# Optimization experiments

Hardware: AMD Instinct MI355X
Metric: run time of the kernel (lower is better)

## Reference

```python
import jax, jax.numpy as jnp
import numpy as np

NUM_STAGES = 8
NUM_CODEBOOKS = 1024  # 2**10
DATA_DIM = 256
T = 131072


def setup_inputs() -> dict:
    key = jax.random.key(0)
    k_x, k_cb = jax.random.split(key)
    input_data = jax.random.normal(k_x, (T, DATA_DIM), dtype=jnp.float32)
    # torch init: Uniform(-1/K, 1/K) per stage
    bound = 1.0 / NUM_CODEBOOKS
    codebooks = jax.random.uniform(
        k_cb, (NUM_STAGES, NUM_CODEBOOKS, DATA_DIM), dtype=jnp.float32,
        minval=-bound, maxval=bound)
    return {"input_data": input_data, "codebooks": codebooks}


def _hard_vq(residual, cb):
    dists = (jnp.sum(residual * residual, axis=1, keepdims=True)
             - 2.0 * (residual @ cb.T)
             + jnp.sum(cb * cb, axis=1)[None, :])
    idx = jnp.argmin(dists, axis=1)          # [T]
    q = cb[idx]                               # gather -> [T, D]
    return q, residual - q, idx


def reference(input_data, codebooks):
    # eval path: stage_map=None (mask of ones), train_mode=False
    residual = input_data
    recon = jnp.zeros_like(input_data)
    mses = []
    for i in range(codebooks.shape[0]):  # fixed small stage loop
        q, residual, _ = _hard_vq(residual, codebooks[i])
        recon = recon + q  # intermediate reconstruction = cumulative sum of q
        mses.append(jnp.mean((recon - input_data) ** 2))
    final_output = recon
    return final_output, jnp.stack(mses)
```

## Files before the change

kernel.cpp:

```cpp
#include <hip/hip_runtime.h>
#include <stdint.h>


#define T_ROWS   131072
#define DIM      256
#define NSTAGE   8
#define NCB      1024
#define WROWS    64
#define BLK_ROWS 256
#define NTHREADS 256
#define CHUNK_CW 32
#define NCHUNK   (NCB / CHUNK_CW)
#define CHUNK_BYTES (CHUNK_CW * 512)

#define WS_CB_BYTES    (NSTAGE * NCB * 512)
#define WS_CNORM_OFF   WS_CB_BYTES
#define WS_CNORM_BYTES (NSTAGE * NCB * 4)
#define WS_MSE_OFF     (WS_CNORM_OFF + WS_CNORM_BYTES)
#define WS_IDX_OFF     (WS_MSE_OFF + 64)

typedef __attribute__((ext_vector_type(8)))  short  s16x8;
typedef __attribute__((ext_vector_type(8)))  __bf16 bf16x8;
typedef __attribute__((ext_vector_type(4)))  float  f32x4;
typedef __attribute__((ext_vector_type(16))) float  f32x16;

__device__ __forceinline__ unsigned short f2bf(float f) {
  union { float f; unsigned u; } v; v.f = f;
  unsigned r = v.u + 0x7FFFu + ((v.u >> 16) & 1u);
  return (unsigned short)(r >> 16);
}

__global__ void vq_prep(const float* __restrict__ CB, char* __restrict__ wscb,
                        float* __restrict__ cnorm) {
  const int tid = threadIdx.x;
  const int cwl = tid >> 5;
  const int j   = tid & 31;
  const int cw  = blockIdx.x * 8 + cwl;
  const int c   = cw & (NCB - 1);
  const float* src = CB + (size_t)cw * DIM + 8 * j;
  f32x4 a = *(const f32x4*)(src);
  f32x4 b = *(const f32x4*)(src + 4);
  s16x8 h;
#pragma unroll
  for (int e = 0; e < 4; ++e) { h[e] = (short)f2bf(a[e]); h[4 + e] = (short)f2bf(b[e]); }
  float sq = a[0]*a[0] + a[1]*a[1] + a[2]*a[2] + a[3]*a[3]
           + b[0]*b[0] + b[1]*b[1] + b[2]*b[2] + b[3]*b[3];
#pragma unroll
  for (int m = 1; m <= 16; m <<= 1) sq += __shfl_xor(sq, m);
  *(s16x8*)(wscb + (size_t)cw * 512 + ((16 * j) ^ ((c & 31) << 4))) = h;
  if (j == 0) cnorm[cw] = sq;
}

__global__ __launch_bounds__(NTHREADS, 2)
void vq_search(const float* __restrict__ X,
               const char* __restrict__ wscb, const float* __restrict__ cnorm,
               unsigned short* __restrict__ IDX, float* __restrict__ wsmse) {
  __shared__ __align__(16) char  lds_cb[3][CHUNK_BYTES];
  __shared__ __align__(16) float lds_cn[NCB];
  __shared__ int   lds_idx[BLK_ROWS];
  __shared__ float lds_n[BLK_ROWS];

  const int tid  = threadIdx.x;
  const int wave = tid >> 6;
  const int lane = tid & 63;
  const int c32  = lane & 31;
  const int hi   = lane >> 5;

  const int rowbase = blockIdx.x * BLK_ROWS + wave * WROWS;

  bf16x8 af[2][16];
  float  sq[2];
#pragma unroll
  for (int t = 0; t < 2; ++t) {
    const float* px = X + (size_t)(rowbase + t * 32 + c32) * DIM + 8 * hi;
    float s2 = 0.f;
#pragma unroll
    for (int s = 0; s < 16; ++s) {
      f32x4 a = *(const f32x4*)(px + 16 * s);
      f32x4 b = *(const f32x4*)(px + 16 * s + 4);
      bf16x8 tt;
#pragma unroll
      for (int e = 0; e < 4; ++e) {
        tt[e] = (__bf16)a[e]; tt[4 + e] = (__bf16)b[e];
        s2 += a[e] * a[e] + b[e] * b[e];
      }
      af[t][s] = tt;
    }
    sq[t] = s2;
  }
#pragma unroll
  for (int t = 0; t < 2; ++t) {
    float v = sq[t] + __shfl_xor(sq[t], 32);
    if (lane < 32) lds_n[wave * WROWS + t * 32 + c32] = v;
  }

  __builtin_amdgcn_global_load_lds(
      (const __attribute__((address_space(1))) char*)((const char*)cnorm + wave * 1024 + lane * 16),
      (__attribute__((address_space(3))) char*)((char*)lds_cn + wave * 1024),
      16, 0, 0);
#pragma unroll
  for (int ch = 0; ch < 2; ++ch)
#pragma unroll
    for (int i = 0; i < 4; ++i) {
      const int seg = (wave * 4 + i) * 1024;
      __builtin_amdgcn_global_load_lds(
          (const __attribute__((address_space(1))) char*)(wscb + (size_t)ch * CHUNK_BYTES + seg + lane * 16),
          (__attribute__((address_space(3))) char*)(&lds_cb[ch][0] + seg),
          16, 0, 0);
    }

  const int swz = c32 << 4;

#pragma unroll 1
  for (int st = 0; st < NSTAGE; ++st) {
    float mv0[16], mv1[16];
#pragma unroll
    for (int r = 0; r < 16; ++r) { mv0[r] = -3.402823466e38f; mv1[r] = -3.402823466e38f; }

    const char* stage_cb = wscb + (size_t)st * NCB * 512;

#pragma unroll 1
    for (int ch = 0; ch < NCHUNK; ++ch) {
      const int cur = ch % 3;

      if (ch + 2 < NCHUNK) {
        const int nx = (ch + 2) % 3;
        const char* src = stage_cb + (size_t)(ch + 2) * CHUNK_BYTES;
#pragma unroll
        for (int i = 0; i < 4; ++i) {
          const int seg = (wave * 4 + i) * 1024;
          __builtin_amdgcn_global_load_lds(
              (const __attribute__((address_space(1))) char*)(src + seg + lane * 16),
              (__attribute__((address_space(3))) char*)(&lds_cb[nx][0] + seg),
              16, 0, 0);
        }
        asm volatile("s_waitcnt vmcnt(8)" ::: "memory");
      } else if (ch + 1 < NCHUNK) {
        asm volatile("s_waitcnt vmcnt(4)" ::: "memory");
      } else {
        asm volatile("s_waitcnt vmcnt(0)" ::: "memory");
      }
      __builtin_amdgcn_sched_barrier(0);
      __builtin_amdgcn_s_barrier();
      __builtin_amdgcn_sched_barrier(0);

      const float cn = lds_cn[ch * CHUNK_CW + c32];
      const float ci = -0.5f * cn;
      f32x16 acc0, acc1;
#pragma unroll
      for (int r = 0; r < 16; ++r) { acc0[r] = ci; acc1[r] = ci; }

      const char* buf = &lds_cb[cur][0];
#pragma unroll
      for (int s = 0; s < 16; ++s) {
        bf16x8 b = *(const bf16x8*)(buf + c32 * 512 + ((s * 32 + hi * 16) ^ swz));
        acc0 = __builtin_amdgcn_mfma_f32_32x32x16_bf16(af[0][s], b, acc0, 0, 0, 0);
        acc1 = __builtin_amdgcn_mfma_f32_32x32x16_bf16(af[1][s], b, acc1, 0, 0, 0);
      }

      const unsigned col = (unsigned)(ch * CHUNK_CW + c32);
#pragma unroll
      for (int r = 0; r < 16; ++r) {
        union { float f; unsigned u; } p0, p1;
        p0.f = acc0[r]; p0.u = (p0.u & 0xFFFFFC00u) | col;
        p1.f = acc1[r]; p1.u = (p1.u & 0xFFFFFC00u) | col;
        mv0[r] = fmaxf(mv0[r], p0.f);
        mv1[r] = fmaxf(mv1[r], p1.f);
      }
      __builtin_amdgcn_sched_barrier(0);
      __builtin_amdgcn_s_barrier();
    }

    float msum = 0.f;
#pragma unroll
    for (int t = 0; t < 2; ++t)
#pragma unroll
      for (int r = 0; r < 16; ++r) {
        float v = (t == 0) ? mv0[r] : mv1[r];
#pragma unroll
        for (int m = 1; m <= 16; m <<= 1) v = fmaxf(v, __shfl_xor(v, m));
        union { float f; unsigned u; } w; w.f = v;
        const float vtrue = __builtin_bit_cast(float, w.u & 0xFFFFFC00u);
        const int   row   = t * 32 + (r & 3) + 8 * (r >> 2) + 4 * hi;
        const int   wrow  = wave * WROWS + row;
        const float n_new = lds_n[wrow] - 2.0f * vtrue;
        msum += n_new;
        if (c32 == 0) {
          lds_n[wrow]   = n_new;
          const int ix = (int)(w.u & 1023u);
          lds_idx[wrow] = ix;
          IDX[st * T_ROWS + rowbase + row] = (unsigned short)ix;
        }
      }
    msum += __shfl_xor(msum, 32);
    if (lane == 0) atomicAdd(wsmse + st, msum);

    if (st != NSTAGE - 1) {
      const char* ncb = stage_cb + (size_t)NCB * 512;
      const char* ncn = (const char*)cnorm + (size_t)(st + 1) * NCB * 4;
      __builtin_amdgcn_global_load_lds(
          (const __attribute__((address_space(1))) char*)(ncn + wave * 1024 + lane * 16),
          (__attribute__((address_space(3))) char*)((char*)lds_cn + wave * 1024),
          16, 0, 0);
#pragma unroll
      for (int ch = 0; ch < 2; ++ch)
#pragma unroll
        for (int i = 0; i < 4; ++i) {
          const int seg = (wave * 4 + i) * 1024;
          __builtin_amdgcn_global_load_lds(
              (const __attribute__((address_space(1))) char*)(ncb + (size_t)ch * CHUNK_BYTES + seg + lane * 16),
              (__attribute__((address_space(3))) char*)(&lds_cb[ch][0] + seg),
              16, 0, 0);
        }

#pragma unroll
      for (int t = 0; t < 2; ++t) {
        const int idx = lds_idx[wave * WROWS + t * 32 + c32];
        const char* q = stage_cb + (size_t)idx * 512;
        const int swzu = (idx & 31) << 4;
#pragma unroll
        for (int s = 0; s < 16; ++s) {
          bf16x8 qb = *(const bf16x8*)(q + ((s * 32 + hi * 16) ^ swzu));
          bf16x8 tt = af[t][s];
#pragma unroll
          for (int e = 0; e < 8; ++e)
            tt[e] = (__bf16)((float)tt[e] - (float)qb[e]);
          af[t][s] = tt;
        }
      }
    }
  }
}

__global__ __launch_bounds__(256)
void vq_recon(const char* __restrict__ wscb, const unsigned short* __restrict__ IDX,
              float* __restrict__ OUT) {
  const int tid = threadIdx.x;
  const int row = blockIdx.x * (256 / 8) + (tid >> 3);
  const int g   = tid & 7;

  int idxs[NSTAGE];
#pragma unroll
  for (int st = 0; st < NSTAGE; ++st) idxs[st] = IDX[st * T_ROWS + row];

  float a[32];
#pragma unroll
  for (int d = 0; d < 32; ++d) a[d] = 0.f;

#pragma unroll
  for (int st = 0; st < NSTAGE; ++st) {
    const char* q = wscb + ((size_t)st * NCB + idxs[st]) * 512;
    const int swzu = (idxs[st] & 31) << 4;
#pragma unroll
    for (int k = 0; k < 4; ++k) {
      bf16x8 qb = *(const bf16x8*)(q + ((g * 64 + 16 * k) ^ swzu));
#pragma unroll
      for (int e = 0; e < 8; ++e) a[k * 8 + e] += (float)qb[e];
    }
  }

  float* po = OUT + (size_t)row * DIM + g * 32;
#pragma unroll
  for (int m = 0; m < 8; ++m) {
    f32x4 o = {a[4 * m], a[4 * m + 1], a[4 * m + 2], a[4 * m + 3]};
    *(f32x4*)(po + 4 * m) = o;
  }
}

__global__ void vq_fin(const float* __restrict__ wsmse, float* __restrict__ OUT) {
  const int i = threadIdx.x;
  if (i < NSTAGE) {
    OUT[(size_t)T_ROWS * DIM + i] = wsmse[i] * (1.0f / ((float)T_ROWS * (float)DIM));
  }
}

extern "C" void kernel_launch(void* const* d_in, const int* in_sizes, int n_in,
                              void* d_out, int out_size, void* d_ws, size_t ws_size,
                              hipStream_t stream) {
  (void)in_sizes; (void)n_in; (void)out_size; (void)ws_size;
  const float* X  = (const float*)d_in[0];
  const float* CB = (const float*)d_in[1];
  float* OUT = (float*)d_out;
  char*  wscb  = (char*)d_ws;
  float* cnorm = (float*)((char*)d_ws + WS_CNORM_OFF);
  float* wsmse = (float*)((char*)d_ws + WS_MSE_OFF);
  unsigned short* IDX = (unsigned short*)((char*)d_ws + WS_IDX_OFF);

  hipMemsetAsync(wsmse, 0, NSTAGE * sizeof(float), stream);
  hipLaunchKernelGGL(vq_prep, dim3((NSTAGE * NCB) / 8), dim3(256), 0, stream,
                     CB, wscb, cnorm);
  hipLaunchKernelGGL(vq_search, dim3(T_ROWS / BLK_ROWS), dim3(NTHREADS), 0, stream,
                     X, wscb, cnorm, IDX, wsmse);
  hipLaunchKernelGGL(vq_recon, dim3(T_ROWS / (256 / 8)), dim3(256), 0, stream,
                     wscb, IDX, OUT);
  hipLaunchKernelGGL(vq_fin, dim3(1), dim3(64), 0, stream, wsmse, OUT);
}
```

Before: 718.6 us.

## Restructure VQ search to 8 waves of 32 rows with 4-buffer single-barrier pipeline

Each wave now handles 32 rows instead of 64, and the block grows to 8 waves. The codebook chunk ring goes from 3 to 4 LDS buffers, with prefetch issued after the MFMA loop so only one barrier is needed per chunk. MFMA sections get raised scheduling priority. Per-stage MSE partials are reduced in LDS so each block issues one atomic instead of one per wave, and the residual update moves before the next-stage prefetch. The aim is more waves in flight to hide LDS and global latency and fewer barriers, at the cost of halving codebook reuse per LDS read (one MFMA per B-fragment load instead of two).

```diff
diff --git a/kernel.cpp b/kernel.cpp
--- a/kernel.cpp
+++ b/kernel.cpp
@@ -6,12 +6,14 @@
 #define DIM      256
 #define NSTAGE   8
 #define NCB      1024
-#define WROWS    64
-#define BLK_ROWS 256
-#define NTHREADS 256
+#define WROWS    32
+#define NWAVE    8
+#define BLK_ROWS (NWAVE * WROWS)
+#define NTHREADS (NWAVE * 64)
 #define CHUNK_CW 32
 #define NCHUNK   (NCB / CHUNK_CW)
 #define CHUNK_BYTES (CHUNK_CW * 512)
+#define NBUF     4
 
 #define WS_CB_BYTES    (NSTAGE * NCB * 512)
 #define WS_CNORM_OFF   WS_CB_BYTES
@@ -51,14 +53,15 @@
   if (j == 0) cnorm[cw] = sq;
 }
 
-__global__ __launch_bounds__(NTHREADS, 2)
+__global__ __launch_bounds__(NTHREADS, 4)
 void vq_search(const float* __restrict__ X,
                const char* __restrict__ wscb, const float* __restrict__ cnorm,
                unsigned short* __restrict__ IDX, float* __restrict__ wsmse) {
-  __shared__ __align__(16) char  lds_cb[3][CHUNK_BYTES];
+  __shared__ __align__(16) char  lds_cb[NBUF][CHUNK_BYTES];
   __shared__ __align__(16) float lds_cn[NCB];
-  __shared__ int   lds_idx[BLK_ROWS];
+  __shared__ unsigned short lds_idx[BLK_ROWS];
   __shared__ float lds_n[BLK_ROWS];
+  __shared__ float lds_msum[NWAVE];
 
   const int tid  = threadIdx.x;
   const int wave = tid >> 6;
@@ -68,11 +71,9 @@
 
   const int rowbase = blockIdx.x * BLK_ROWS + wave * WROWS;
 
-  bf16x8 af[2][16];
-  float  sq[2];
-#pragma unroll
-  for (int t = 0; t < 2; ++t) {
-    const float* px = X + (size_t)(rowbase + t * 32 + c32) * DIM + 8 * hi;
+  bf16x8 af[16];
+  {
+    const float* px = X + (size_t)(rowbase + c32) * DIM + 8 * hi;
     float s2 = 0.f;
 #pragma unroll
     for (int s = 0; s < 16; ++s) {
@@ -84,25 +85,22 @@
         tt[e] = (__bf16)a[e]; tt[4 + e] = (__bf16)b[e];
         s2 += a[e] * a[e] + b[e] * b[e];
       }
-      af[t][s] = tt;
-    }
-    sq[t] = s2;
-  }
-#pragma unroll
-  for (int t = 0; t < 2; ++t) {
-    float v = sq[t] + __shfl_xor(sq[t], 32);
-    if (lane < 32) lds_n[wave * WROWS + t * 32 + c32] = v;
-  }
-
-  __builtin_amdgcn_global_load_lds(
-      (const __attribute__((address_space(1))) char*)((const char*)cnorm + wave * 1024 + lane * 16),
-      (__attribute__((address_space(3))) char*)((char*)lds_cn + wave * 1024),
-      16, 0, 0);
-#pragma unroll
-  for (int ch = 0; ch < 2; ++ch)
-#pragma unroll
-    for (int i = 0; i < 4; ++i) {
-      const int seg = (wave * 4 + i) * 1024;
+      af[s] = tt;
+    }
+    float v = s2 + __shfl_xor(s2, 32);
+    if (lane < 32) lds_n[wave * WROWS + c32] = v;
+  }
+
+  if (wave < 4)
+    __builtin_amdgcn_global_load_lds(
+        (const __attribute__((address_space(1))) char*)((const char*)cnorm + wave * 1024 + lane * 16),
+        (__attribute__((address_space(3))) char*)((char*)lds_cn + wave * 1024),
+        16, 0, 0);
+#pragma unroll
+  for (int ch = 0; ch < 3; ++ch)
+#pragma unroll
+    for (int i = 0; i < 2; ++i) {
+      const int seg = (wave * 2 + i) * 1024;
       __builtin_amdgcn_global_load_lds(
           (const __attribute__((address_space(1))) char*)(wscb + (size_t)ch * CHUNK_BYTES + seg + lane * 16),
           (__attribute__((address_space(3))) char*)(&lds_cb[ch][0] + seg),
@@ -113,30 +111,20 @@
 
 #pragma unroll 1
   for (int st = 0; st < NSTAGE; ++st) {
-    float mv0[16], mv1[16];
-#pragma unroll
-    for (int r = 0; r < 16; ++r) { mv0[r] = -3.402823466e38f; mv1[r] = -3.402823466e38f; }
+    float mv[16];
+#pragma unroll
+    for (int r = 0; r < 16; ++r) mv[r] = -3.402823466e38f;
 
     const char* stage_cb = wscb + (size_t)st * NCB * 512;
 
 #pragma unroll 1
     for (int ch = 0; ch < NCHUNK; ++ch) {
-      const int cur = ch % 3;
-
-      if (ch + 2 < NCHUNK) {
-        const int nx = (ch + 2) % 3;
-        const char* src = stage_cb + (size_t)(ch + 2) * CHUNK_BYTES;
-#pragma unroll
-        for (int i = 0; i < 4; ++i) {
-          const int seg = (wave * 4 + i) * 1024;
-          __builtin_amdgcn_global_load_lds(
-              (const __attribute__((address_space(1))) char*)(src + seg + lane * 16),
-              (__attribute__((address_space(3))) char*)(&lds_cb[nx][0] + seg),
-              16, 0, 0);
-        }
-        asm volatile("s_waitcnt vmcnt(8)" ::: "memory");
-      } else if (ch + 1 < NCHUNK) {
+      const int cur = ch & (NBUF - 1);
+
+      if (ch < NCHUNK - 2) {
         asm volatile("s_waitcnt vmcnt(4)" ::: "memory");
+      } else if (ch == NCHUNK - 2) {
+        asm volatile("s_waitcnt vmcnt(2)" ::: "memory");
       } else {
         asm volatile("s_waitcnt vmcnt(0)" ::: "memory");
       }
@@ -144,90 +132,110 @@
       __builtin_amdgcn_s_barrier();
       __builtin_amdgcn_sched_barrier(0);
 
-      const float cn = lds_cn[ch * CHUNK_CW + c32];
-      const float ci = -0.5f * cn;
-      f32x16 acc0, acc1;
-#pragma unroll
-      for (int r = 0; r < 16; ++r) { acc0[r] = ci; acc1[r] = ci; }
+      const float cnv = lds_cn[ch * CHUNK_CW + c32];
+      f32x16 acc;
+#pragma unroll
+      for (int r = 0; r < 16; ++r) acc[r] = 0.f;
 
       const char* buf = &lds_cb[cur][0];
+      __builtin_amdgcn_s_setprio(1);
 #pragma unroll
       for (int s = 0; s < 16; ++s) {
         bf16x8 b = *(const bf16x8*)(buf + c32 * 512 + ((s * 32 + hi * 16) ^ swz));
-        acc0 = __builtin_amdgcn_mfma_f32_32x32x16_bf16(af[0][s], b, acc0, 0, 0, 0);
-        acc1 = __builtin_amdgcn_mfma_f32_32x32x16_bf16(af[1][s], b, acc1, 0, 0, 0);
-      }
-
+        acc = __builtin_amdgcn_mfma_f32_32x32x16_bf16(af[s], b, acc, 0, 0, 0);
+      }
+      __builtin_amdgcn_s_setprio(0);
+
+      if (ch + 3 < NCHUNK) {
+        const char* src = stage_cb + (size_t)(ch + 3) * CHUNK_BYTES;
+        char* dst = &lds_cb[(ch + 3) & (NBUF - 1)][0];
+#pragma unroll
+        for (int i = 0; i < 2; ++i) {
+          const int seg = (wave * 2 + i) * 1024;
+          __builtin_amdgcn_global_load_lds(
+              (const __attribute__((address_space(1))) char*)(src + seg + lane * 16),
+              (__attribute__((address_space(3))) char*)(dst + seg),
+              16, 0, 0);
+        }
+      }
+
+      const float cnh = 0.5f * cnv;
       const unsigned col = (unsigned)(ch * CHUNK_CW + c32);
 #pragma unroll
       for (int r = 0; r < 16; ++r) {
-        union { float f; unsigned u; } p0, p1;
-        p0.f = acc0[r]; p0.u = (p0.u & 0xFFFFFC00u) | col;
-        p1.f = acc1[r]; p1.u = (p1.u & 0xFFFFFC00u) | col;
-        mv0[r] = fmaxf(mv0[r], p0.f);
-        mv1[r] = fmaxf(mv1[r], p1.f);
-      }
-      __builtin_amdgcn_sched_barrier(0);
-      __builtin_amdgcn_s_barrier();
+        union { float f; unsigned u; } p;
+        p.f = acc[r] - cnh;
+        p.u = (p.u & 0xFFFFFC00u) | col;
+        mv[r] = fmaxf(mv[r], p.f);
+      }
     }
 
     float msum = 0.f;
 #pragma unroll
-    for (int t = 0; t < 2; ++t)
-#pragma unroll
-      for (int r = 0; r < 16; ++r) {
-        float v = (t == 0) ? mv0[r] : mv1[r];
-#pragma unroll
-        for (int m = 1; m <= 16; m <<= 1) v = fmaxf(v, __shfl_xor(v, m));
-        union { float f; unsigned u; } w; w.f = v;
-        const float vtrue = __builtin_bit_cast(float, w.u & 0xFFFFFC00u);
-        const int   row   = t * 32 + (r & 3) + 8 * (r >> 2) + 4 * hi;
-        const int   wrow  = wave * WROWS + row;
-        const float n_new = lds_n[wrow] - 2.0f * vtrue;
-        msum += n_new;
-        if (c32 == 0) {
-          lds_n[wrow]   = n_new;
-          const int ix = (int)(w.u & 1023u);
-          lds_idx[wrow] = ix;
-          IDX[st * T_ROWS + rowbase + row] = (unsigned short)ix;
-        }
-      }
+    for (int r = 0; r < 16; ++r) {
+      float v = mv[r];
+#pragma unroll
+      for (int m = 1; m <= 16; m <<= 1) v = fmaxf(v, __shfl_xor(v, m));
+      union { float f; unsigned u; } w; w.f = v;
+      const float vtrue = __builtin_bit_cast(float, w.u & 0xFFFFFC00u);
+      const int   row   = (r & 3) + 8 * (r >> 2) + 4 * hi;
+      const int   wrow  = wave * WROWS + row;
+      const float n_new = lds_n[wrow] - 2.0f * vtrue;
+      msum += n_new;
+      if (c32 == 0) {
+        lds_n[wrow]   = n_new;
+        const int ix = (int)(w.u & 1023u);
+        lds_idx[wrow] = (unsigned short)ix;
+        IDX[st * T_ROWS + rowbase + row] = (unsigned short)ix;
+      }
+    }
     msum += __shfl_xor(msum, 32);
-    if (lane == 0) atomicAdd(wsmse + st, msum);
+    if (lane == 0) lds_msum[wave] = msum;
+
+    if (st != NSTAGE - 1) {
+      const int idx = (int)lds_idx[wave * WROWS + c32];
+      const char* q = stage_cb + (size_t)idx * 512;
+      const int swzu = (idx & 31) << 4;
+#pragma unroll
+      for (int s = 0; s < 16; ++s) {
+        bf16x8 qb = *(const bf16x8*)(q + ((s * 32 + hi * 16) ^ swzu));
+        bf16x8 tt = af[s];
+#pragma unroll
+        for (int e = 0; e < 8; ++e)
+          tt[e] = (__bf16)((float)tt[e] - (float)qb[e]);
+        af[s] = tt;
+      }
+    }
+
+    __builtin_amdgcn_sched_barrier(0);
+    __builtin_amdgcn_s_barrier();
+    __builtin_amdgcn_sched_barrier(0);
+
+    if (wave == 0) {
+      float v = (lane < NWAVE) ? lds_msum[lane] : 0.f;
+#pragma unroll
+      for (int m = 1; m < NWAVE; m <<= 1) v += __shfl_xor(v, m);
+      if (lane == 0) atomicAdd(wsmse + st, v);
+    }
 
     if (st != NSTAGE - 1) {
       const char* ncb = stage_cb + (size_t)NCB * 512;
       const char* ncn = (const char*)cnorm + (size_t)(st + 1) * NCB * 4;
-      __builtin_amdgcn_global_load_lds(
-          (const __attribute__((address_space(1))) char*)(ncn + wave * 1024 + lane * 16),
-          (__attribute__((address_space(3))) char*)((char*)lds_cn + wave * 1024),
-          16, 0, 0);
-#pragma unroll
-      for (int ch = 0; ch < 2; ++ch)
-#pragma unroll
-        for (int i = 0; i < 4; ++i) {
-          const int seg = (wave * 4 + i) * 1024;
+      if (wave < 4)
+        __builtin_amdgcn_global_load_lds(
+            (const __attribute__((address_space(1))) char*)(ncn + wave * 1024 + lane * 16),
+            (__attribute__((address_space(3))) char*)((char*)lds_cn + wave * 1024),
+            16, 0, 0);
+#pragma unroll
+      for (int ch = 0; ch < 3; ++ch)
+#pragma unroll
+        for (int i = 0; i < 2; ++i) {
+          const int seg = (wave * 2 + i) * 1024;
           __builtin_amdgcn_global_load_lds(
               (const __attribute__((address_space(1))) char*)(ncb + (size_t)ch * CHUNK_BYTES + seg + lane * 16),
               (__attribute__((address_space(3))) char*)(&lds_cb[ch][0] + seg),
               16, 0, 0);
         }
-
-#pragma unroll
-      for (int t = 0; t < 2; ++t) {
-        const int idx = lds_idx[wave * WROWS + t * 32 + c32];
-        const char* q = stage_cb + (size_t)idx * 512;
-        const int swzu = (idx & 31) << 4;
-#pragma unroll
-        for (int s = 0; s < 16; ++s) {
-          bf16x8 qb = *(const bf16x8*)(q + ((s * 32 + hi * 16) ^ swzu));
-          bf16x8 tt = af[t][s];
-#pragma unroll
-          for (int e = 0; e < 8; ++e)
-            tt[e] = (__bf16)((float)tt[e] - (float)qb[e]);
-          af[t][s] = tt;
-        }
-      }
     }
   }
 }
```

New measurement: 700.8 us. -2.5%, faster.
